# Kernel tuning notes

Measured on AMD Instinct MI355X. Metric: run time of the kernel, lower is better.

## Reference

```python
import jax, jax.numpy as jnp
import numpy as np

N_NODES = 50000
N_EDGES = 1600000
D_IN = 128
D_OUT = 128
EPS = 0.001  # GINConv(eps=0.001) hard-coded in the module


def setup_inputs() -> dict:
    key = jax.random.key(0)
    k_x, k_e, k_w1, k_b1, k_w2, k_b2 = jax.random.split(key, 6)
    x = jax.random.normal(k_x, (N_NODES, D_IN), dtype=jnp.float32)
    edge_index = jax.random.randint(k_e, (2, N_EDGES), 0, N_NODES, dtype=jnp.int64)
    # MLP params (nn.Linear default init scale ~ 1/sqrt(fan_in))
    s1 = 1.0 / np.sqrt(D_IN)
    s2 = 1.0 / np.sqrt(D_OUT)
    W1 = jax.random.uniform(k_w1, (D_IN, D_OUT), jnp.float32, -s1, s1)
    b1 = jax.random.uniform(k_b1, (D_OUT,), jnp.float32, -s1, s1)
    W2 = jax.random.uniform(k_w2, (D_OUT, D_OUT), jnp.float32, -s2, s2)
    b2 = jax.random.uniform(k_b2, (D_OUT,), jnp.float32, -s2, s2)
    return {"x": x, "edge_index": edge_index, "W1": W1, "b1": b1, "W2": W2, "b2": b2}


def reference(x, edge_index, W1, b1, W2, b2):
    # GIN: out = MLP((1 + eps) * x + sum_{j in N(i)} x_j)
    src = edge_index[0]  # message source nodes
    dst = edge_index[1]  # aggregation targets
    agg = jax.ops.segment_sum(x[src], dst, num_segments=x.shape[0])  # [N, D_IN]
    h = (1.0 + EPS) * x + agg
    h = jax.nn.relu(h @ W1 + b1)
    return h @ W2 + b2
```

## Files before the change

kernel.cpp:

```cpp
#include <hip/hip_runtime.h>
#include <hip/hip_bf16.h>


#define N_NODES 50000
#define N_EDGES 1600000
#define D 128

#define MMB 391
#define SCH 4096
#define NSB 391
#define BSH 6
#define BSZ 64
#define KB 782
#define CAPB 2560
#define HP 136

typedef __attribute__((ext_vector_type(8))) short short8;
typedef __attribute__((ext_vector_type(4))) float float4v;

__device__ inline unsigned short f2b(float f) {
    unsigned u = __builtin_bit_cast(unsigned, f);
    u = u + 0x7fffu + ((u >> 16) & 1u);
    return (unsigned short)(u >> 16);
}
__device__ inline float b2f_lo(unsigned u) { return __builtin_bit_cast(float, u << 16); }
__device__ inline float b2f_hi(unsigned u) { return __builtin_bit_cast(float, u & 0xffff0000u); }

__global__ __launch_bounds__(1024) void k_prep(const float* __restrict__ W1,
                                               const float* __restrict__ W2,
                                               unsigned short* __restrict__ Wt1,
                                               unsigned short* __restrict__ Wt2,
                                               unsigned* __restrict__ bpos,
                                               const int* __restrict__ ei,
                                               int* __restrict__ flag) {
    int bb = blockIdx.x;
    if (bb == 0) {
        __shared__ int nz;
        if (threadIdx.x == 0) nz = 0;
        __syncthreads();
        if (threadIdx.x < 256 && ei[threadIdx.x * 2 + 1] != 0) atomicAdd(&nz, 1);
        __syncthreads();
        if (threadIdx.x == 0) *flag = (nz == 0) ? 1 : 0;
        for (int i = threadIdx.x; i < KB; i += 1024) bpos[i] = 0u;
    }
    const float* W = (bb < 4) ? W1 : W2;
    unsigned short* Wt = (bb < 4) ? Wt1 : Wt2;
    int q = bb & 3;
    for (int i = q * 4096 + threadIdx.x; i < (q + 1) * 4096; i += 1024) {
        int k = i >> 7;
        int n = i & 127;
        Wt[n * 128 + k] = f2b(W[k * 128 + n]);
    }
}

__global__ __launch_bounds__(512) void k_mmsort(const float* __restrict__ x,
                                                const unsigned short* __restrict__ Wt1g,
                                                unsigned short* __restrict__ y,
                                                const int* __restrict__ ei,
                                                const int* __restrict__ flag,
                                                unsigned* __restrict__ bpos,
                                                unsigned* __restrict__ pairs) {
    __shared__ unsigned hist[KB];
    int bid = blockIdx.x;
    int t = threadIdx.x;

    if (bid < MMB) {
        int row0 = bid * 128;
        int w = t >> 6;
        int lane = t & 63;
        int quad = lane >> 4;
        int l16 = lane & 15;
        int arow = row0 + w * 16 + l16;
        const float* xrow = x + (size_t)arow * 128;

        float4v acc[8];
        #pragma unroll
        for (int nt = 0; nt < 8; ++nt) acc[nt] = (float4v){0.f, 0.f, 0.f, 0.f};

        #pragma unroll
        for (int kc = 0; kc < 4; ++kc) {
            int koff = kc * 32 + quad * 8;
            float4 v0 = make_float4(0.f, 0.f, 0.f, 0.f);
            float4 v1 = make_float4(0.f, 0.f, 0.f, 0.f);
            if (arow < N_NODES) {
                v0 = *(const float4*)&xrow[koff];
                v1 = *(const float4*)&xrow[koff + 4];
            }
            short8 a;
            a[0] = (short)f2b(v0.x); a[1] = (short)f2b(v0.y);
            a[2] = (short)f2b(v0.z); a[3] = (short)f2b(v0.w);
            a[4] = (short)f2b(v1.x); a[5] = (short)f2b(v1.y);
            a[6] = (short)f2b(v1.z); a[7] = (short)f2b(v1.w);
            #pragma unroll
            for (int nt = 0; nt < 8; ++nt) {
                short8 bfr = *(const short8*)&Wt1g[(nt * 16 + l16) * 128 + koff];
                acc[nt] = __builtin_amdgcn_mfma_f32_16x16x32_bf16(a, bfr, acc[nt], 0, 0, 0);
            }
        }
        #pragma unroll
        for (int nt = 0; nt < 8; ++nt) {
            int col = nt * 16 + l16;
            #pragma unroll
            for (int r = 0; r < 4; ++r) {
                int grow = row0 + w * 16 + quad * 4 + r;
                if (grow < N_NODES)
                    y[(size_t)grow * 128 + col] = f2b(acc[nt][r]);
            }
        }
        return;
    }

    int b = bid - MMB;
    for (int i = t; i < KB; i += 512) hist[i] = 0u;
    __syncthreads();
    int wide = *flag;
    int e0 = b * SCH + t * 8;
    int dv[8], sv[8], rv[8];
    if (e0 < N_EDGES) {
        if (wide) {
            const uint4* pd = (const uint4*)&ei[((size_t)N_EDGES + e0) * 2];
            const uint4* ps = (const uint4*)&ei[(size_t)e0 * 2];
            #pragma unroll
            for (int j = 0; j < 4; ++j) {
                uint4 qd = pd[j], qs = ps[j];
                dv[2 * j] = (int)qd.x; dv[2 * j + 1] = (int)qd.z;
                sv[2 * j] = (int)qs.x; sv[2 * j + 1] = (int)qs.z;
            }
        } else {
            const uint4* pd = (const uint4*)&ei[(size_t)N_EDGES + e0];
            const uint4* ps = (const uint4*)&ei[e0];
            #pragma unroll
            for (int j = 0; j < 2; ++j) {
                uint4 qd = pd[j], qs = ps[j];
                dv[4 * j] = (int)qd.x; dv[4 * j + 1] = (int)qd.y;
                dv[4 * j + 2] = (int)qd.z; dv[4 * j + 3] = (int)qd.w;
                sv[4 * j] = (int)qs.x; sv[4 * j + 1] = (int)qs.y;
                sv[4 * j + 2] = (int)qs.z; sv[4 * j + 3] = (int)qs.w;
            }
        }
    } else {
        #pragma unroll
        for (int i = 0; i < 8; ++i) dv[i] = -1;
    }
    #pragma unroll
    for (int i = 0; i < 8; ++i) {
        if ((unsigned)dv[i] < (unsigned)N_NODES) {
            rv[i] = (int)atomicAdd(&hist[dv[i] >> BSH], 1u);
            if ((unsigned)sv[i] >= (unsigned)N_NODES) sv[i] = 0;
        } else dv[i] = -1;
    }
    __syncthreads();
    for (int i = t; i < KB; i += 512) {
        unsigned c = hist[i];
        hist[i] = c ? atomicAdd(&bpos[i], c) : 0u;
    }
    __syncthreads();
    #pragma unroll
    for (int i = 0; i < 8; ++i) {
        if (dv[i] >= 0) {
            int kb = dv[i] >> BSH;
            unsigned r = hist[kb] + (unsigned)rv[i];
            if (r < CAPB)
                pairs[(size_t)kb * CAPB + r] =
                    (unsigned)sv[i] | ((unsigned)(dv[i] & (BSZ - 1)) << 17);
        }
    }
}

__global__ __launch_bounds__(512) void k_bgather(const unsigned short* __restrict__ y,
                                                 const unsigned* __restrict__ pairs,
                                                 const unsigned* __restrict__ bpos,
                                                 const float* __restrict__ b1,
                                                 const unsigned short* __restrict__ Wt2g,
                                                 const float* __restrict__ b2,
                                                 float* __restrict__ out) {
    __shared__ unsigned sbuf[CAPB];
    __shared__ short htile[BSZ * HP];
    __shared__ int cnt[BSZ], loff[BSZ], pos[BSZ];
    int k = blockIdx.x;
    int t = threadIdx.x;
    if (t < BSZ) cnt[t] = 0;
    __syncthreads();
    int beg = k * CAPB;
    int tot = (int)bpos[k];
    if (tot > CAPB) tot = CAPB;
    for (int i = t; i < tot; i += 512)
        atomicAdd(&cnt[pairs[beg + i] >> 17], 1);
    __syncthreads();
    if (t < BSZ) {
        int v = cnt[t];
        int xs = v;
        #pragma unroll
        for (int off = 1; off < 64; off <<= 1) {
            int u0 = __shfl_up(xs, off, 64);
            if (t >= off) xs += u0;
        }
        loff[t] = xs - v;
        pos[t] = xs - v;
    }
    __syncthreads();
    for (int i = t; i < tot; i += 512) {
        unsigned p = pairs[beg + i];
        int r = atomicAdd(&pos[p >> 17], 1);
        sbuf[r] = p & 0x1FFFFu;
    }
    __syncthreads();

    int w = t >> 6;
    int lane = t & 63;
    int g = lane >> 5;
    int u = lane & 31;
    const uint2* yr = (const uint2*)y;

    #pragma unroll 1
    for (int q = 0; q < 8; ++q) {
        int dl = w * 8 + q;
        int node = (k << BSH) + dl;
        int jb = loff[dl];
        int je = jb + cnt[dl];
        float a0 = 0.f, a1 = 0.f, a2 = 0.f, a3 = 0.f;
        int j = jb + g;
        for (; j + 14 < je; j += 16) {
            int ss[8];
            #pragma unroll
            for (int q2 = 0; q2 < 8; ++q2) ss[q2] = (int)sbuf[j + 2 * q2];
            #pragma unroll
            for (int q2 = 0; q2 < 8; ++q2) {
                uint2 A = yr[(size_t)ss[q2] * 32 + u];
                a0 += b2f_lo(A.x); a1 += b2f_hi(A.x);
                a2 += b2f_lo(A.y); a3 += b2f_hi(A.y);
            }
        }
        for (; j < je; j += 2) {
            uint2 A = yr[(size_t)sbuf[j] * 32 + u];
            a0 += b2f_lo(A.x); a1 += b2f_hi(A.x);
            a2 += b2f_lo(A.y); a3 += b2f_hi(A.y);
        }
        a0 += __shfl_xor(a0, 32, 64); a1 += __shfl_xor(a1, 32, 64);
        a2 += __shfl_xor(a2, 32, 64); a3 += __shfl_xor(a3, 32, 64);
        if (g == 0) {
            uint2 o = make_uint2(0u, 0u);
            if (node < N_NODES) {
                uint2 S = yr[(size_t)node * 32 + u];
                float4 bv = ((const float4*)b1)[u];
                float f0 = fmaf(1.001f, b2f_lo(S.x), a0) + bv.x;
                float f1 = fmaf(1.001f, b2f_hi(S.x), a1) + bv.y;
                float f2 = fmaf(1.001f, b2f_lo(S.y), a2) + bv.z;
                float f3 = fmaf(1.001f, b2f_hi(S.y), a3) + bv.w;
                f0 = fmaxf(f0, 0.f); f1 = fmaxf(f1, 0.f);
                f2 = fmaxf(f2, 0.f); f3 = fmaxf(f3, 0.f);
                o.x = (unsigned)f2b(f0) | ((unsigned)f2b(f1) << 16);
                o.y = (unsigned)f2b(f2) | ((unsigned)f2b(f3) << 16);
            }
            *(uint2*)&htile[dl * HP + u * 4] = o;
        }
    }
    __syncthreads();

    int quad = lane >> 4;
    int l16 = lane & 15;
    int mt = w >> 1;
    int nh = w & 1;
    float4v accB[4];
    #pragma unroll
    for (int nt2 = 0; nt2 < 4; ++nt2) accB[nt2] = (float4v){0.f, 0.f, 0.f, 0.f};
    #pragma unroll
    for (int kc = 0; kc < 4; ++kc) {
        int koff = kc * 32 + quad * 8;
        short8 a = *(const short8*)&htile[(mt * 16 + l16) * HP + koff];
        #pragma unroll
        for (int nt2 = 0; nt2 < 4; ++nt2) {
            int col = nh * 64 + nt2 * 16 + l16;
            short8 bfr = *(const short8*)&Wt2g[col * 128 + koff];
            accB[nt2] = __builtin_amdgcn_mfma_f32_16x16x32_bf16(a, bfr, accB[nt2], 0, 0, 0);
        }
    }
    int node0 = k << BSH;
    #pragma unroll
    for (int nt2 = 0; nt2 < 4; ++nt2) {
        int col = nh * 64 + nt2 * 16 + l16;
        float bb = b2[col];
        #pragma unroll
        for (int r = 0; r < 4; ++r) {
            int grow = node0 + mt * 16 + quad * 4 + r;
            if (grow < N_NODES)
                out[(size_t)grow * 128 + col] = accB[nt2][r] + bb;
        }
    }
}

extern "C" void kernel_launch(void* const* d_in, const int* in_sizes, int n_in,
                              void* d_out, int out_size, void* d_ws, size_t ws_size,
                              hipStream_t stream) {
    const float* x  = (const float*)d_in[0];
    const int*   ei = (const int*)d_in[1];
    const float* W1 = (const float*)d_in[2];
    const float* b1 = (const float*)d_in[3];
    const float* W2 = (const float*)d_in[4];
    const float* b2 = (const float*)d_in[5];
    float* out = (float*)d_out;

    char* ws = (char*)d_ws;
    unsigned short* y       = (unsigned short*)(ws);
    unsigned*       pairs   = (unsigned*)(ws + 12800000);
    unsigned*       bpos    = (unsigned*)(ws + 21000000);
    unsigned short* Wt1     = (unsigned short*)(ws + 21100000);
    unsigned short* Wt2     = (unsigned short*)(ws + 21200000);
    int*            flag    = (int*)    (ws + 21300000);

    k_prep<<<8, 1024, 0, stream>>>(W1, W2, Wt1, Wt2, bpos, ei, flag);
    k_mmsort<<<MMB + NSB, 512, 0, stream>>>(x, Wt1, y, ei, flag, bpos, pairs);
    k_bgather<<<KB, 512, 0, stream>>>(y, pairs, bpos, b1, Wt2, b2, out);
}
```

Baseline: 199.4 us.

## Stage W1 in padded LDS, interleave matmul and sort blocks, widen prep

The matmul blocks now copy the bf16 W1 tile into padded shared memory and read B fragments from LDS instead of global memory. Matmul and edge-sort blocks are interleaved by block parity so both workloads are spread across CUs at the same time, and the two share one shared-memory buffer. The weight transpose in the prep kernel runs on 32 blocks with one element per thread and coalesced writes. Zeroing bpos moves to a memset. This raises LDS use per block (about 34 KB), which may lower occupancy for the sort blocks.

```diff
diff --git a/kernel.cpp b/kernel.cpp
--- a/kernel.cpp
+++ b/kernel.cpp
@@ -14,6 +14,7 @@
 #define KB 782
 #define CAPB 2560
 #define HP 136
+#define LPAD 136
 
 typedef __attribute__((ext_vector_type(8))) short short8;
 typedef __attribute__((ext_vector_type(4))) float float4v;
@@ -30,7 +31,6 @@
                                                const float* __restrict__ W2,
                                                unsigned short* __restrict__ Wt1,
                                                unsigned short* __restrict__ Wt2,
-                                               unsigned* __restrict__ bpos,
                                                const int* __restrict__ ei,
                                                int* __restrict__ flag) {
     int bb = blockIdx.x;
@@ -41,16 +41,14 @@
         if (threadIdx.x < 256 && ei[threadIdx.x * 2 + 1] != 0) atomicAdd(&nz, 1);
         __syncthreads();
         if (threadIdx.x == 0) *flag = (nz == 0) ? 1 : 0;
-        for (int i = threadIdx.x; i < KB; i += 1024) bpos[i] = 0u;
-    }
-    const float* W = (bb < 4) ? W1 : W2;
-    unsigned short* Wt = (bb < 4) ? Wt1 : Wt2;
-    int q = bb & 3;
-    for (int i = q * 4096 + threadIdx.x; i < (q + 1) * 4096; i += 1024) {
-        int k = i >> 7;
-        int n = i & 127;
-        Wt[n * 128 + k] = f2b(W[k * 128 + n]);
-    }
+    }
+    const float* W = (bb < 16) ? W1 : W2;
+    unsigned short* Wt = (bb < 16) ? Wt1 : Wt2;
+    int q = (bb < 16) ? bb : bb - 16;
+    int i = q * 1024 + threadIdx.x;
+    int n = i >> 7;
+    int k = i & 127;
+    Wt[i] = f2b(W[k * 128 + n]);
 }
 
 __global__ __launch_bounds__(512) void k_mmsort(const float* __restrict__ x,
@@ -60,12 +58,24 @@
                                                 const int* __restrict__ flag,
                                                 unsigned* __restrict__ bpos,
                                                 unsigned* __restrict__ pairs) {
-    __shared__ unsigned hist[KB];
+    __shared__ short smem[128 * LPAD];
     int bid = blockIdx.x;
     int t = threadIdx.x;
 
-    if (bid < MMB) {
-        int row0 = bid * 128;
+    if ((bid & 1) == 0) {
+        int row0 = (bid >> 1) * 128;
+        {
+            const uint4* Wg4 = (const uint4*)Wt1g;
+            #pragma unroll
+            for (int i = 0; i < 4; ++i) {
+                int idx = i * 512 + t;
+                int r = idx >> 4;
+                int c = idx & 15;
+                *(uint4*)&smem[r * LPAD + c * 8] = Wg4[idx];
+            }
+        }
+        __syncthreads();
+
         int w = t >> 6;
         int lane = t & 63;
         int quad = lane >> 4;
@@ -93,7 +103,7 @@
             a[6] = (short)f2b(v1.z); a[7] = (short)f2b(v1.w);
             #pragma unroll
             for (int nt = 0; nt < 8; ++nt) {
-                short8 bfr = *(const short8*)&Wt1g[(nt * 16 + l16) * 128 + koff];
+                short8 bfr = *(const short8*)&smem[(nt * 16 + l16) * LPAD + koff];
                 acc[nt] = __builtin_amdgcn_mfma_f32_16x16x32_bf16(a, bfr, acc[nt], 0, 0, 0);
             }
         }
@@ -110,7 +120,8 @@
         return;
     }
 
-    int b = bid - MMB;
+    unsigned* hist = (unsigned*)smem;
+    int b = bid >> 1;
     for (int i = t; i < KB; i += 512) hist[i] = 0u;
     __syncthreads();
     int wide = *flag;
@@ -308,7 +319,8 @@
     unsigned short* Wt2     = (unsigned short*)(ws + 21200000);
     int*            flag    = (int*)    (ws + 21300000);
 
-    k_prep<<<8, 1024, 0, stream>>>(W1, W2, Wt1, Wt2, bpos, ei, flag);
+    hipMemsetAsync(bpos, 0, KB * sizeof(unsigned), stream);
+    k_prep<<<32, 1024, 0, stream>>>(W1, W2, Wt1, Wt2, ei, flag);
     k_mmsort<<<MMB + NSB, 512, 0, stream>>>(x, Wt1, y, ei, flag, bpos, pairs);
     k_bgather<<<KB, 512, 0, stream>>>(y, pairs, bpos, b1, Wt2, b2, out);
 }
```

After: 190.9 us. 4.3% less time.
